# Kernel optimization log

Measured on AMD Instinct MI355X. Metric: run time of the kernel, lower is better.

Reference implementation:

```python
import jax, jax.numpy as jnp
import numpy as np

I = 18   # input_size
H = 18   # hidden_size
L = 2    # num_layers
B = 4096
T = 512


def setup_inputs() -> dict:
    key = jax.random.key(0)
    ks = jax.random.split(key, 9)
    s = 1.0 / np.sqrt(H)  # PyTorch LSTM init scale
    inp = {"x": jax.random.normal(ks[0], (B, T, I), dtype=jnp.float32)}
    # Layer 0: input size I; Layer 1: input size H. Gate order i,f,g,o (PyTorch).
    inp["w_ih0"] = jax.random.uniform(ks[1], (4 * H, I), jnp.float32, -s, s)
    inp["w_hh0"] = jax.random.uniform(ks[2], (4 * H, H), jnp.float32, -s, s)
    inp["b_ih0"] = jax.random.uniform(ks[3], (4 * H,), jnp.float32, -s, s)
    inp["b_hh0"] = jax.random.uniform(ks[4], (4 * H,), jnp.float32, -s, s)
    inp["w_ih1"] = jax.random.uniform(ks[5], (4 * H, H), jnp.float32, -s, s)
    inp["w_hh1"] = jax.random.uniform(ks[6], (4 * H, H), jnp.float32, -s, s)
    inp["b_ih1"] = jax.random.uniform(ks[7], (4 * H,), jnp.float32, -s, s)
    inp["b_hh1"] = jax.random.uniform(ks[8], (4 * H,), jnp.float32, -s, s)
    return inp


def _lstm_layer(x_tbd, w_ih, w_hh, b_ih, b_hh):
    # x_tbd: [T, B, D_in]; zero initial (h, c) as in the torch module.
    b = b_ih + b_hh
    # Precompute input projection for all timesteps: [T, B, 4H]
    x_proj = jnp.einsum('tbd,gd->tbg', x_tbd, w_ih) + b
    h0 = jnp.zeros((x_tbd.shape[1], H), x_tbd.dtype)
    c0 = jnp.zeros((x_tbd.shape[1], H), x_tbd.dtype)

    def step(carry, xp):
        h, c = carry
        gates = xp + h @ w_hh.T  # [B, 4H]
        i, f, g, o = jnp.split(gates, 4, axis=-1)
        i = jax.nn.sigmoid(i)
        f = jax.nn.sigmoid(f)
        g = jnp.tanh(g)
        o = jax.nn.sigmoid(o)
        c = f * c + i * g
        h = o * jnp.tanh(c)
        return (h, c), h

    _, hs = jax.lax.scan(step, (h0, c0), x_proj)
    return hs  # [T, B, H]


def reference(x, w_ih0, w_hh0, b_ih0, b_hh0, w_ih1, w_hh1, b_ih1, b_hh1):
    x_tbd = jnp.transpose(x, (1, 0, 2))  # [T, B, I]
    h1 = _lstm_layer(x_tbd, w_ih0, w_hh0, b_ih0, b_hh0)
    h2 = _lstm_layer(h1, w_ih1, w_hh1, b_ih1, b_hh1)
    return jnp.transpose(h2, (1, 0, 2))  # [B, T, H]
```

## Files before the change

kernel.cpp:

```cpp
#include <hip/hip_runtime.h>

#define TT   512
#define HD   18
#define NB   16
#define NTH  256
#define RS   68

typedef _Float16 v8h __attribute__((ext_vector_type(8)));
typedef float    v4f __attribute__((ext_vector_type(4)));

__device__ __forceinline__ float fsig(float x) {
    return __builtin_amdgcn_rcpf(1.0f + __expf(-x));
}

__device__ __forceinline__ void softbar() {
    asm volatile("s_waitcnt lgkmcnt(0)" ::: "memory");
    __builtin_amdgcn_s_barrier();
    __builtin_amdgcn_sched_barrier(0);
}


template<int NT>
__device__ __forceinline__ void run_wave(
    int tbase, int isl1, int pfmode, int lane,
    const float* __restrict__ x,
    const float* __restrict__ wih, const float* __restrict__ whh,
    const float* __restrict__ bi,  const float* __restrict__ bh,
    float* __restrict__ out,
    _Float16 (*SH)[NB][RS], size_t b0)
{
    const int rl = lane & 15;
    const int lg = lane >> 4;

    v8h Af[NT][2];
    int hh[NT];
    #pragma unroll
    for (int i = 0; i < NT; ++i) {
        const int row = 16 * (tbase + i) + rl;
        const int h = row >> 2, g = row & 3;
        const int r = g * HD + h;
        #pragma unroll
        for (int s = 0; s < 2; ++s) {
            v8h a;
            #pragma unroll
            for (int j = 0; j < 8; ++j) {
                const int k = 8 * lg + j + 32 * s;
                float v = 0.f;
                if (h < HD) {
                    if (k < HD)            v = wih[r * HD + k];
                    else if (k < 2 * HD)   v = whh[r * HD + (k - HD)];
                    else if (k == 2 * HD)  v = bi[r] + bh[r];
                }
                a[j] = (_Float16)v;
            }
            Af[i][s] = a;
        }
        hh[i] = 4 * (tbase + i) + lg;
    }

    float* op[NT];
    #pragma unroll
    for (int i = 0; i < NT; ++i)
        op[i] = out + (b0 + rl) * (size_t)TT * HD + hh[i];

    int pb[3] = {0,0,0}, pk[3] = {0,0,0}; bool pv[3] = {false,false,false};
    float xpf[3] = {0.f, 0.f, 0.f};
    if (pfmode) {
        int ee[3];
        ee[0] = (pfmode == 1) ? lane       : 128 + lane;
        ee[1] = (pfmode == 1) ? 64 + lane  : 192 + lane;
        ee[2] = (pfmode == 1) ? 256 + lane : 999;
        #pragma unroll
        for (int j = 0; j < 3; ++j) {
            pv[j] = ee[j] < NB * HD;
            pb[j] = pv[j] ? ee[j] / HD : 0;
            pk[j] = pv[j] ? ee[j] % HD : 0;
            if (pv[j])
                xpf[j] = x[(b0 + pb[j]) * (size_t)TT * HD + 3 * HD + pk[j]];
        }
    }

    float cst[NT];
    #pragma unroll
    for (int i = 0; i < NT; ++i) cst[i] = 0.f;

    for (int n = 0; n <= TT; ++n) {
        float xnew[3] = {0.f, 0.f, 0.f};
        if (pfmode && (n + 4) < TT) {
            #pragma unroll
            for (int j = 0; j < 3; ++j)
                if (pv[j]) xnew[j] = x[(b0 + pb[j]) * (size_t)TT * HD
                                       + (size_t)(n + 4) * HD + pk[j]];
        }

        const bool active = isl1 ? (n < TT) : (n >= 1);
        if (active) {
            const int bufi = isl1 ? (n & 3) : (4 + (n & 1));
            const _Float16* rowp = &SH[bufi][rl][0];
            v8h Bf[2];
            #pragma unroll
            for (int s = 0; s < 2; ++s) {
                union { uint2 u[2]; v8h v; } cv;
                cv.u[0] = *(const uint2*)(rowp + 8 * lg + 32 * s);
                cv.u[1] = *(const uint2*)(rowp + 8 * lg + 32 * s + 4);
                Bf[s] = cv.v;
            }
            const int wb1 = (n + 1) & 3;
            const int wb2 = 4 + ((n + 1) & 1);
            #pragma unroll
            for (int i = 0; i < NT; ++i) {
                v4f acc = {0.f, 0.f, 0.f, 0.f};
                acc = __builtin_amdgcn_mfma_f32_16x16x32_f16(Af[i][0], Bf[0], acc, 0, 0, 0);
                acc = __builtin_amdgcn_mfma_f32_16x16x32_f16(Af[i][1], Bf[1], acc, 0, 0, 0);
                const float gi = fsig(acc[0]);
                const float gf = fsig(acc[1]);
                const float gg = 2.f * fsig(2.f * acc[2]) - 1.f;
                const float go = fsig(acc[3]);
                cst[i] = gf * cst[i] + gi * gg;
                const float th = 2.f * fsig(2.f * cst[i]) - 1.f;
                const float hv = go * th;
                const _Float16 h16 = (_Float16)hv;
                if (hh[i] < HD) {
                    if (isl1) {
                        SH[wb1][rl][HD + hh[i]] = h16;
                        SH[wb2][rl][hh[i]]      = h16;
                    } else {
                        SH[wb2][rl][HD + hh[i]] = h16;
                        op[i][(size_t)(n - 1) * HD] = hv;
                    }
                }
            }
        }
        if (pfmode) {
            if (n + 3 < TT) {
                const int xb = (n + 3) & 3;
                #pragma unroll
                for (int j = 0; j < 3; ++j)
                    if (pv[j]) SH[xb][pb[j]][pk[j]] = (_Float16)xpf[j];
            }
            #pragma unroll
            for (int j = 0; j < 3; ++j) xpf[j] = xnew[j];
        }
        softbar();
    }
}

__global__ __launch_bounds__(NTH) void lstm2_mfma_nb(
    const float* __restrict__ x,
    const float* __restrict__ wih0, const float* __restrict__ whh0,
    const float* __restrict__ bih0, const float* __restrict__ bhh0,
    const float* __restrict__ wih1, const float* __restrict__ whh1,
    const float* __restrict__ bih1, const float* __restrict__ bhh1,
    float* __restrict__ out)
{
    __shared__ __align__(16) _Float16 SH[6][NB][RS];

    const int tid  = threadIdx.x;
    const int wid  = tid >> 6;
    const int lane = tid & 63;
    const size_t b0 = (size_t)blockIdx.x * NB;

    {
        uint* shw = (uint*)&SH[0][0][0];
        for (int i = tid; i < 6 * NB * RS / 2; i += NTH) shw[i] = 0u;
        __syncthreads();
        for (int i = tid; i < 6 * NB; i += NTH)
            SH[i / NB][i % NB][2 * HD] = (_Float16)1.0f;
        for (int i = tid; i < 3 * NB * HD; i += NTH) {
            const int t = i / (NB * HD), r2 = i % (NB * HD);
            const int b = r2 / HD, k = r2 % HD;
            SH[t][b][k] = (_Float16)x[(b0 + b) * (size_t)TT * HD + t * HD + k];
        }
        __syncthreads();
    }

    if      (wid == 0) run_wave<3>(0, 1, 0, lane, x, wih0, whh0, bih0, bhh0, out, SH, b0);
    else if (wid == 1) run_wave<2>(3, 1, 1, lane, x, wih0, whh0, bih0, bhh0, out, SH, b0);
    else if (wid == 2) run_wave<3>(0, 0, 0, lane, x, wih1, whh1, bih1, bhh1, out, SH, b0);
    else               run_wave<2>(3, 0, 2, lane, x, wih1, whh1, bih1, bhh1, out, SH, b0);
}

extern "C" void kernel_launch(void* const* d_in, const int* in_sizes, int n_in,
                              void* d_out, int out_size, void* d_ws, size_t ws_size,
                              hipStream_t stream) {
    const float* x    = (const float*)d_in[0];
    const float* wih0 = (const float*)d_in[1];
    const float* whh0 = (const float*)d_in[2];
    const float* bih0 = (const float*)d_in[3];
    const float* bhh0 = (const float*)d_in[4];
    const float* wih1 = (const float*)d_in[5];
    const float* whh1 = (const float*)d_in[6];
    const float* bih1 = (const float*)d_in[7];
    const float* bhh1 = (const float*)d_in[8];
    float* out = (float*)d_out;
    (void)d_ws; (void)ws_size; (void)in_sizes; (void)n_in; (void)out_size;

    lstm2_mfma_nb<<<dim3(4096 / NB), dim3(NTH), 0, stream>>>(
        x, wih0, whh0, bih0, bhh0, wih1, whh1, bih1, bhh1, out);
}
```

Measured before the change: 297.2 us.

## Split input projections into dedicated producer waves pipelined with recurrent waves

Adds two extra waves per block that compute the input projections (x·W_ih0 and h1·W_ih1 plus bias) one step ahead and stage them in LDS as fp32 gate pre-activations. The recurrent waves then need one K=32 MFMA instead of two per tile, seeded with the staged values, which shortens the serial per-step critical path. The layer pipeline is now skewed over TT+3 barrier steps. Cost: 384 threads per block, more LDS for the gate buffers, and extra barrier participants.

```diff
diff --git a/kernel.cpp b/kernel.cpp
--- a/kernel.cpp
+++ b/kernel.cpp
@@ -3,8 +3,9 @@
 #define TT   512
 #define HD   18
 #define NB   16
-#define NTH  256
-#define RS   68
+#define NTH  384
+#define HRS  40
+#define GRS  20
 
 typedef _Float16 v8h __attribute__((ext_vector_type(8)));
 typedef float    v4f __attribute__((ext_vector_type(4)));
@@ -16,102 +17,91 @@
 __device__ __forceinline__ void softbar() {
     asm volatile("s_waitcnt lgkmcnt(0)" ::: "memory");
     __builtin_amdgcn_s_barrier();
-    __builtin_amdgcn_sched_barrier(0);
-}
-
-
-template<int NT>
-__device__ __forceinline__ void run_wave(
-    int tbase, int isl1, int pfmode, int lane,
-    const float* __restrict__ x,
-    const float* __restrict__ wih, const float* __restrict__ whh,
-    const float* __restrict__ bi,  const float* __restrict__ bh,
-    float* __restrict__ out,
-    _Float16 (*SH)[NB][RS], size_t b0)
+    asm volatile("" ::: "memory");
+}
+
+template<bool PROJ>
+__device__ __forceinline__ v8h build_A(int tile, int rl, int lg,
+                                       const float* __restrict__ wm,
+                                       const float* __restrict__ bi,
+                                       const float* __restrict__ bh)
 {
-    const int rl = lane & 15;
-    const int lg = lane >> 4;
-
-    v8h Af[NT][2];
+    const int row = 16 * tile + rl;
+    const int h = row >> 2, g = row & 3;
+    const int r = g * HD + h;
+    v8h a;
+    #pragma unroll
+    for (int j = 0; j < 8; ++j) {
+        const int k = 8 * lg + j;
+        float v = 0.f;
+        if (h < HD) {
+            if (k < HD)               v = wm[r * HD + k];
+            else if (PROJ && k == HD) v = bi[r] + bh[r];
+        }
+        a[j] = (_Float16)v;
+    }
+    return a;
+}
+
+__device__ __forceinline__ void load_x2(const float* __restrict__ base, int lg, float2* d) {
+    if (lg < 2) {
+        d[0] = *(const float2*)(base + 0);
+        d[1] = *(const float2*)(base + 2);
+        d[2] = *(const float2*)(base + 4);
+        d[3] = *(const float2*)(base + 6);
+    } else if (lg == 2) {
+        d[0] = *(const float2*)(base + 0);
+    }
+}
+
+__device__ __forceinline__ v8h pack_x(const float2* s, int lg) {
+    v8h b;
+    #pragma unroll
+    for (int j = 0; j < 8; ++j) b[j] = (_Float16)0.f;
+    if (lg < 2) {
+        b[0] = (_Float16)s[0].x; b[1] = (_Float16)s[0].y;
+        b[2] = (_Float16)s[1].x; b[3] = (_Float16)s[1].y;
+        b[4] = (_Float16)s[2].x; b[5] = (_Float16)s[2].y;
+        b[6] = (_Float16)s[3].x; b[7] = (_Float16)s[3].y;
+    } else if (lg == 2) {
+        b[0] = (_Float16)s[0].x; b[1] = (_Float16)s[0].y;
+        b[2] = (_Float16)1.0f;
+    }
+    return b;
+}
+
+template<int NT, bool ISL1>
+__device__ __forceinline__ void rec_wave(
+    int tbase, int lane,
+    const float* __restrict__ whh,
+    float* __restrict__ out, size_t b0,
+    _Float16 (*hs)[NB][HRS],
+    const float (*gs)[5][NB][GRS])
+{
+    const int rl = lane & 15, lg = lane >> 4;
+    v8h A[NT];
     int hh[NT];
+    float cst[NT];
     #pragma unroll
     for (int i = 0; i < NT; ++i) {
-        const int row = 16 * (tbase + i) + rl;
-        const int h = row >> 2, g = row & 3;
-        const int r = g * HD + h;
-        #pragma unroll
-        for (int s = 0; s < 2; ++s) {
-            v8h a;
-            #pragma unroll
-            for (int j = 0; j < 8; ++j) {
-                const int k = 8 * lg + j + 32 * s;
-                float v = 0.f;
-                if (h < HD) {
-                    if (k < HD)            v = wih[r * HD + k];
-                    else if (k < 2 * HD)   v = whh[r * HD + (k - HD)];
-                    else if (k == 2 * HD)  v = bi[r] + bh[r];
-                }
-                a[j] = (_Float16)v;
-            }
-            Af[i][s] = a;
-        }
+        A[i] = build_A<false>(tbase + i, rl, lg, whh, nullptr, nullptr);
         hh[i] = 4 * (tbase + i) + lg;
-    }
-
-    float* op[NT];
-    #pragma unroll
-    for (int i = 0; i < NT; ++i)
-        op[i] = out + (b0 + rl) * (size_t)TT * HD + hh[i];
-
-    int pb[3] = {0,0,0}, pk[3] = {0,0,0}; bool pv[3] = {false,false,false};
-    float xpf[3] = {0.f, 0.f, 0.f};
-    if (pfmode) {
-        int ee[3];
-        ee[0] = (pfmode == 1) ? lane       : 128 + lane;
-        ee[1] = (pfmode == 1) ? 64 + lane  : 192 + lane;
-        ee[2] = (pfmode == 1) ? 256 + lane : 999;
-        #pragma unroll
-        for (int j = 0; j < 3; ++j) {
-            pv[j] = ee[j] < NB * HD;
-            pb[j] = pv[j] ? ee[j] / HD : 0;
-            pk[j] = pv[j] ? ee[j] % HD : 0;
-            if (pv[j])
-                xpf[j] = x[(b0 + pb[j]) * (size_t)TT * HD + 3 * HD + pk[j]];
-        }
-    }
-
-    float cst[NT];
-    #pragma unroll
-    for (int i = 0; i < NT; ++i) cst[i] = 0.f;
-
-    for (int n = 0; n <= TT; ++n) {
-        float xnew[3] = {0.f, 0.f, 0.f};
-        if (pfmode && (n + 4) < TT) {
-            #pragma unroll
-            for (int j = 0; j < 3; ++j)
-                if (pv[j]) xnew[j] = x[(b0 + pb[j]) * (size_t)TT * HD
-                                       + (size_t)(n + 4) * HD + pk[j]];
-        }
-
-        const bool active = isl1 ? (n < TT) : (n >= 1);
-        if (active) {
-            const int bufi = isl1 ? (n & 3) : (4 + (n & 1));
-            const _Float16* rowp = &SH[bufi][rl][0];
-            v8h Bf[2];
-            #pragma unroll
-            for (int s = 0; s < 2; ++s) {
-                union { uint2 u[2]; v8h v; } cv;
-                cv.u[0] = *(const uint2*)(rowp + 8 * lg + 32 * s);
-                cv.u[1] = *(const uint2*)(rowp + 8 * lg + 32 * s + 4);
-                Bf[s] = cv.v;
-            }
-            const int wb1 = (n + 1) & 3;
-            const int wb2 = 4 + ((n + 1) & 1);
+        cst[i] = 0.f;
+    }
+    float* op = out + (b0 + rl) * (size_t)TT * HD;
+
+    constexpr int lo = ISL1 ? 1 : 3;
+    constexpr int hi = ISL1 ? TT : TT + 2;
+
+    for (int n = 0; n <= TT + 2; ++n) {
+        if (n >= lo && n <= hi) {
+            const _Float16* hrow = &hs[n & 1][rl][0];
+            const v8h B = *(const v8h*)(hrow + 8 * lg);
+            const int wp = (n + 1) & 1;
             #pragma unroll
             for (int i = 0; i < NT; ++i) {
-                v4f acc = {0.f, 0.f, 0.f, 0.f};
-                acc = __builtin_amdgcn_mfma_f32_16x16x32_f16(Af[i][0], Bf[0], acc, 0, 0, 0);
-                acc = __builtin_amdgcn_mfma_f32_16x16x32_f16(Af[i][1], Bf[1], acc, 0, 0, 0);
+                v4f acc = *(const v4f*)&gs[wp][tbase + i][rl][4 * lg];
+                acc = __builtin_amdgcn_mfma_f32_16x16x32_f16(A[i], B, acc, 0, 0, 0);
                 const float gi = fsig(acc[0]);
                 const float gf = fsig(acc[1]);
                 const float gg = 2.f * fsig(2.f * acc[2]) - 1.f;
@@ -119,33 +109,18 @@
                 cst[i] = gf * cst[i] + gi * gg;
                 const float th = 2.f * fsig(2.f * cst[i]) - 1.f;
                 const float hv = go * th;
-                const _Float16 h16 = (_Float16)hv;
                 if (hh[i] < HD) {
-                    if (isl1) {
-                        SH[wb1][rl][HD + hh[i]] = h16;
-                        SH[wb2][rl][hh[i]]      = h16;
-                    } else {
-                        SH[wb2][rl][HD + hh[i]] = h16;
-                        op[i][(size_t)(n - 1) * HD] = hv;
-                    }
+                    hs[wp][rl][hh[i]] = (_Float16)hv;
+                    if (!ISL1)
+                        op[(size_t)(n - 3) * HD + hh[i]] = hv;
                 }
             }
         }
-        if (pfmode) {
-            if (n + 3 < TT) {
-                const int xb = (n + 3) & 3;
-                #pragma unroll
-                for (int j = 0; j < 3; ++j)
-                    if (pv[j]) SH[xb][pb[j]][pk[j]] = (_Float16)xpf[j];
-            }
-            #pragma unroll
-            for (int j = 0; j < 3; ++j) xpf[j] = xnew[j];
-        }
         softbar();
     }
 }
 
-__global__ __launch_bounds__(NTH) void lstm2_mfma_nb(
+__global__ __launch_bounds__(NTH) void lstm2_split(
     const float* __restrict__ x,
     const float* __restrict__ wih0, const float* __restrict__ whh0,
     const float* __restrict__ bih0, const float* __restrict__ bhh0,
@@ -153,31 +128,77 @@
     const float* __restrict__ bih1, const float* __restrict__ bhh1,
     float* __restrict__ out)
 {
-    __shared__ __align__(16) _Float16 SH[6][NB][RS];
+    __shared__ __align__(16) _Float16 h1s[2][NB][HRS];
+    __shared__ __align__(16) _Float16 h2s[2][NB][HRS];
+    __shared__ __align__(16) float    gxs[2][5][NB][GRS];
+    __shared__ __align__(16) float    ghs[2][5][NB][GRS];
 
     const int tid  = threadIdx.x;
     const int wid  = tid >> 6;
     const int lane = tid & 63;
+    const int rl   = lane & 15, lg = lane >> 4;
     const size_t b0 = (size_t)blockIdx.x * NB;
 
     {
-        uint* shw = (uint*)&SH[0][0][0];
-        for (int i = tid; i < 6 * NB * RS / 2; i += NTH) shw[i] = 0u;
+        uint* hw = (uint*)&h1s[0][0][0];
+        for (int i = tid; i < 2 * NB * HRS / 2; i += NTH) hw[i] = 0u;
+        uint* hw2 = (uint*)&h2s[0][0][0];
+        for (int i = tid; i < 2 * NB * HRS / 2; i += NTH) hw2[i] = 0u;
         __syncthreads();
-        for (int i = tid; i < 6 * NB; i += NTH)
-            SH[i / NB][i % NB][2 * HD] = (_Float16)1.0f;
-        for (int i = tid; i < 3 * NB * HD; i += NTH) {
-            const int t = i / (NB * HD), r2 = i % (NB * HD);
-            const int b = r2 / HD, k = r2 % HD;
-            SH[t][b][k] = (_Float16)x[(b0 + b) * (size_t)TT * HD + t * HD + k];
+        for (int i = tid; i < 2 * NB; i += NTH) {
+            h1s[i / NB][i % NB][HD] = (_Float16)1.0f;
+            h2s[i / NB][i % NB][HD] = (_Float16)1.0f;
         }
         __syncthreads();
     }
 
-    if      (wid == 0) run_wave<3>(0, 1, 0, lane, x, wih0, whh0, bih0, bhh0, out, SH, b0);
-    else if (wid == 1) run_wave<2>(3, 1, 1, lane, x, wih0, whh0, bih0, bhh0, out, SH, b0);
-    else if (wid == 2) run_wave<3>(0, 0, 0, lane, x, wih1, whh1, bih1, bhh1, out, SH, b0);
-    else               run_wave<2>(3, 0, 2, lane, x, wih1, whh1, bih1, bhh1, out, SH, b0);
+    if (wid == 0)      rec_wave<3, true >(0, lane, whh0, out, b0, h1s, gxs);
+    else if (wid == 1) rec_wave<2, true >(3, lane, whh0, out, b0, h1s, gxs);
+    else if (wid == 2) rec_wave<3, false>(0, lane, whh1, out, b0, h2s, ghs);
+    else if (wid == 3) rec_wave<2, false>(3, lane, whh1, out, b0, h2s, ghs);
+    else if (wid == 5) {
+        v8h A[5];
+        #pragma unroll
+        for (int i = 0; i < 5; ++i) A[i] = build_A<true>(i, rl, lg, wih1, bih1, bhh1);
+        for (int n = 0; n <= TT + 2; ++n) {
+            if (n >= 2 && n <= TT + 1) {
+                const v8h B = *(const v8h*)(&h1s[n & 1][rl][0] + 8 * lg);
+                const int wp = n & 1;
+                #pragma unroll
+                for (int i = 0; i < 5; ++i) {
+                    v4f acc = {0.f, 0.f, 0.f, 0.f};
+                    acc = __builtin_amdgcn_mfma_f32_16x16x32_f16(A[i], B, acc, 0, 0, 0);
+                    *(v4f*)&ghs[wp][i][rl][4 * lg] = acc;
+                }
+            }
+            softbar();
+        }
+    } else {
+        v8h A[5];
+        #pragma unroll
+        for (int i = 0; i < 5; ++i) A[i] = build_A<true>(i, rl, lg, wih0, bih0, bhh0);
+        const float* xb = x + (b0 + rl) * (size_t)TT * HD + 8 * lg;
+        float2 xe[4], xo[4];
+        load_x2(xb + 0 * HD, lg, xe);
+        load_x2(xb + 1 * HD, lg, xo);
+        for (int n = 0; n <= TT + 2; ++n) {
+            if (n < TT) {
+                const v8h B = (n & 1) ? pack_x(xo, lg) : pack_x(xe, lg);
+                const int wp = n & 1;
+                #pragma unroll
+                for (int i = 0; i < 5; ++i) {
+                    v4f acc = {0.f, 0.f, 0.f, 0.f};
+                    acc = __builtin_amdgcn_mfma_f32_16x16x32_f16(A[i], B, acc, 0, 0, 0);
+                    *(v4f*)&gxs[wp][i][rl][4 * lg] = acc;
+                }
+                if (n + 2 < TT) {
+                    if (n & 1) load_x2(xb + (size_t)(n + 2) * HD, lg, xo);
+                    else       load_x2(xb + (size_t)(n + 2) * HD, lg, xe);
+                }
+            }
+            softbar();
+        }
+    }
 }
 
 extern "C" void kernel_launch(void* const* d_in, const int* in_sizes, int n_in,
@@ -195,6 +216,6 @@
     float* out = (float*)d_out;
     (void)d_ws; (void)ws_size; (void)in_sizes; (void)n_in; (void)out_size;
 
-    lstm2_mfma_nb<<<dim3(4096 / NB), dim3(NTH), 0, stream>>>(
+    lstm2_split<<<dim3(4096 / NB), dim3(NTH), 0, stream>>>(
         x, wih0, whh0, bih0, bhh0, wih1, whh1, bih1, bhh1, out);
 }
```

New measurement: 365.8 us. +23.1%, slower.
